# Kernel optimization log

Measured on AMD Instinct MI355X. Metric: run time of the kernel, lower is better.

## Reference

```python
import jax, jax.numpy as jnp
import numpy as np

D = 300
L = 5
NUM_ATOMS = 87  # MASK_ATOM_ID + 1
BN_EPS = 1e-5


def setup_inputs() -> dict:
    key = jax.random.key(0)
    ks = jax.random.split(key, 24)
    N, E, G = 100000, 250000, 4096
    s = 0.05
    inp = {
        'z': jax.random.randint(ks[0], (N,), 0, 86),
        'chirality': jax.random.uniform(ks[1], (N,), jnp.float32),
        'formal_charge': jax.random.normal(ks[2], (N,), jnp.float32),
        'edge_index': jax.random.randint(ks[3], (2, E), 0, N),
        'edge_attr': jax.random.normal(ks[4], (E, 3), jnp.float32),
        'batch': jnp.sort(jax.random.randint(ks[5], (N,), 0, G)),
        'num_graphs': G,
        # parameters
        'atom_emb': jax.random.normal(ks[6], (NUM_ATOMS, D), jnp.float32) * s,
        'nW1': jax.random.normal(ks[7], (2, D), jnp.float32) * s,
        'nb1': jnp.zeros((D,), jnp.float32),
        'nW2': jax.random.normal(ks[8], (D, D), jnp.float32) * s,
        'nb2': jnp.zeros((D,), jnp.float32),
        'eW1': jax.random.normal(ks[9], (3, D), jnp.float32) * s,
        'eb1': jnp.zeros((D,), jnp.float32),
        'eW2': jax.random.normal(ks[10], (D, D), jnp.float32) * s,
        'eb2': jnp.zeros((D,), jnp.float32),
        'mW1': jax.random.normal(ks[11], (L, D, D), jnp.float32) * s,
        'mb1': jnp.zeros((L, D), jnp.float32),
        'mW2': jax.random.normal(ks[12], (L, D, D), jnp.float32) * s,
        'mb2': jnp.zeros((L, D), jnp.float32),
        'gamma': jnp.ones((L, D), jnp.float32),
        'beta': jnp.zeros((L, D), jnp.float32),
        'pW': jax.random.normal(ks[13], (D, D), jnp.float32) * s,
        'pb': jnp.zeros((D,), jnp.float32),
    }
    return inp


def _mlp2(x, W1, b1, W2, b2):
    return jax.nn.relu(x @ W1 + b1) @ W2 + b2


def reference(z, chirality, formal_charge, edge_index, edge_attr, batch, num_graphs,
              atom_emb, nW1, nb1, nW2, nb2, eW1, eb1, eW2, eb2,
              mW1, mb1, mW2, mb2, gamma, beta, pW, pb):
    N = z.shape[0]
    # node features: atom embedding + projected (chirality, formal_charge)
    node_attr = jnp.stack([chirality, formal_charge], axis=-1)  # [N,2]
    x = atom_emb[z] + _mlp2(node_attr, nW1, nb1, nW2, nb2)      # [N,D]
    # edge features: encode 3-d bond attrs to D (edge_proj is Identity since dims match)
    e = _mlp2(edge_attr, eW1, eb1, eW2, eb2)                    # [E,D]
    src, dst = edge_index[0], edge_index[1]
    h = x
    for l in range(L):
        # GINEConv: mlp((1+eps)*x_i + sum_j relu(x_j + e_ij)), eps=0
        msg = jax.nn.relu(h[src] + e)                           # [E,D] gather
        agg = jax.ops.segment_sum(msg, dst, num_segments=N)     # [N,D] scatter-add
        h2 = _mlp2(h + agg, mW1[l], mb1[l], mW2[l], mb2[l])
        # BatchNorm1d (training stats over nodes, biased var)
        mu = jnp.mean(h2, axis=0)
        var = jnp.var(h2, axis=0)
        h2 = (h2 - mu) * jax.lax.rsqrt(var + BN_EPS) * gamma[l] + beta[l]
        h = jax.nn.relu(h2)
    # per-graph mean pooling
    sums = jax.ops.segment_sum(h, batch, num_segments=num_graphs)      # [G,D]
    counts = jax.ops.segment_sum(jnp.ones((N,), h.dtype), batch, num_segments=num_graphs)
    pooled = sums / jnp.maximum(counts, 1.0)[:, None]
    return pooled @ pW + pb
```

## Files before the change

### kernel.cpp

```cpp
#include <hip/hip_runtime.h>

#define DD 300
#define KP 320
#define WTR 384

typedef __attribute__((ext_vector_type(8))) short short8v;
typedef __attribute__((ext_vector_type(4))) float f32x4;

__device__ __forceinline__ float4 ld4(const float* p) { return *(const float4*)p; }

__device__ __forceinline__ unsigned short f2bf(float f) {
    unsigned int u = __float_as_uint(f);
    unsigned int r = (u + 0x7fffu + ((u >> 16) & 1u)) >> 16;
    return (unsigned short)r;
}
__device__ __forceinline__ float bf2f(unsigned short b) {
    return __uint_as_float(((unsigned int)b) << 16);
}

__device__ __forceinline__ void gload16(const void* g, void* l) {
    __builtin_amdgcn_global_load_lds(
        (const __attribute__((address_space(1))) unsigned int*)g,
        (__attribute__((address_space(3))) unsigned int*)l, 16, 0, 0);
}

__device__ __forceinline__ unsigned char f2e4(float f) {
    unsigned int u = __float_as_uint(f);
    unsigned int s = (u >> 24) & 0x80u;
    float a = __uint_as_float(u & 0x7fffffffu);
    if (a >= 448.f) return (unsigned char)(s | 0x7Eu);
    if (a < 0x1p-10f) return (unsigned char)s;
    int e = (int)((__float_as_uint(a) >> 23) & 0xFF) - 127;
    int q = (e >= -6) ? (e - 3) : -9;
    float scale = __uint_as_float((unsigned int)(127 - q) << 23);
    int m = __float2int_rn(a * scale);
    if (e >= -6) {
        if (m == 16) { m = 8; e += 1; }
        return (unsigned char)(s | ((unsigned int)(e + 7) << 3) | (unsigned int)(m - 8));
    } else {
        if (m == 8) return (unsigned char)(s | (1u << 3));
        return (unsigned char)(s | (unsigned int)m);
    }
}
__device__ __forceinline__ float e42f(unsigned char b) {
    unsigned int s = ((unsigned int)(b & 0x80u)) << 24;
    unsigned int ef = (b >> 3) & 0xFu, mf = b & 7u;
    float mag = (ef == 0) ? ((float)mf) * 0x1p-9f
                          : __uint_as_float(((ef + 120u) << 23) | (mf << 20));
    return __uint_as_float(__float_as_uint(mag) | s);
}

__global__ void prep_all(const float* __restrict__ nW2, const float* __restrict__ eW2,
                         const float* __restrict__ mW1, const float* __restrict__ mW2,
                         unsigned short* __restrict__ wt,
                         double* __restrict__ bnsum, double* __restrict__ bnsq)
{
    const int per = WTR * KP;
    int id = blockIdx.x * 256 + threadIdx.x;
    if (id < 12 * per) {
        int m = id / per, r = id - m * per;
        int col = r / KP, k = r - col * KP;
        const float* W = (m == 0) ? nW2 : (m == 1) ? eW2
                       : (m < 7) ? (mW1 + (size_t)(m - 2) * DD * DD)
                                 : (mW2 + (size_t)(m - 7) * DD * DD);
        float v = (col < DD && k < DD) ? W[(size_t)k * DD + col] : 0.f;
        unsigned short h = f2bf(v);
        wt[(size_t)m * 2 * per + (size_t)col * KP + k] = h;
        wt[(size_t)m * 2 * per + per + (size_t)col * KP + k] = f2bf(v - bf2f(h));
    } else if (id < 12 * per + DD) {
        int c = id - 12 * per;
        bnsum[c] = 0.0; bnsq[c] = 0.0;
    }
}

enum { MA_DMA2 = 0, MA_BF16 = 1, MA_NODE = 2, MA_EDGE = 3 };
enum { ME_RELU = 0, ME_BN = 1, ME_EMB = 2, ME_FP8 = 3 };

constexpr int TM = 128;
constexpr int TN = 128;
constexpr int TK = 32;
constexpr int KSTEPS = 10;

template<int AM, int EM>
__launch_bounds__(256)
__global__ void mgemm(const unsigned short* __restrict__ Aa,
                      const unsigned short* __restrict__ Ab,
                      const unsigned short* __restrict__ Bth,
                      const unsigned short* __restrict__ Btl,
                      const float* __restrict__ bias,
                      const float* __restrict__ W1,
                      const float* __restrict__ b1,
                      const int* __restrict__ zidx,
                      const float* __restrict__ emb,
                      const int* __restrict__ permpos,
                      void* __restrict__ Cv,
                      double* __restrict__ bnsum, double* __restrict__ bnsq,
                      int M)
{
    constexpr bool VSTAGE = (AM == MA_NODE || AM == MA_EDGE);
    constexpr int AP = VSTAGE ? 40 : 32;
    __shared__ unsigned short sAh[TM * AP];
    __shared__ unsigned short sBh[TN * 32];
    __shared__ unsigned short sBl[TN * 32];
    __shared__ unsigned short sA2[(AM == MA_DMA2) ? TM * 32 : 64];
    __shared__ unsigned short sAl[VSTAGE ? TM * 40 : 64];

    const int t    = threadIdx.x;
    const int col0 = blockIdx.x * TN;
    const int row0 = blockIdx.y * TM;
    const int lane = t & 63;
    const int wid  = t >> 6;
    const int wr   = wid >> 1;
    const int wc   = wid & 1;
    const int lr   = lane & 15;
    const int lk   = lane >> 4;

    const int arow = t >> 1;
    const int akq  = (t & 1) * 16;
    const int dmarow = lane >> 2;
    const int dmakq  = (lane & 3) * 8;
    const int wbase  = wid * 32;

    const int ga = row0 + arow;
    float f0 = 0.f, f1 = 0.f, f2 = 0.f;
    if (AM == MA_NODE && ga < M) {
        f0 = ((const float*)Aa)[ga]; f1 = ((const float*)Ab)[ga];
    }
    if (AM == MA_EDGE && ga < M) {
        const float* Af = (const float*)Aa;
        f0 = Af[(size_t)ga * 3 + 0];
        f1 = Af[(size_t)ga * 3 + 1];
        f2 = Af[(size_t)ga * 3 + 2];
    }

    f32x4 acc[4][4];
#pragma unroll
    for (int i = 0; i < 4; ++i)
#pragma unroll
        for (int j = 0; j < 4; ++j) acc[i][j] = (f32x4){0.f, 0.f, 0.f, 0.f};

    for (int ks = 0; ks < KSTEPS; ++ks) {
        const int k0 = ks * TK;
        __syncthreads();

#pragma unroll
        for (int i = 0; i < 2; ++i) {
            const int rb = wbase + i * 16;
            gload16(Bth + (size_t)(col0 + rb + dmarow) * KP + k0 + dmakq, &sBh[rb * 32]);
            gload16(Btl + (size_t)(col0 + rb + dmarow) * KP + k0 + dmakq, &sBl[rb * 32]);
        }

        if (AM == MA_DMA2) {
#pragma unroll
            for (int i = 0; i < 2; ++i) {
                const int rb = wbase + i * 16;
                gload16(Aa + (size_t)(row0 + rb + dmarow) * DD + k0 + dmakq, &sAh[rb * 32]);
                gload16(Ab + (size_t)(row0 + rb + dmarow) * DD + k0 + dmakq, &sA2[rb * 32]);
            }
        } else if (AM == MA_BF16) {
#pragma unroll
            for (int i = 0; i < 2; ++i) {
                const int rb = wbase + i * 16;
                gload16(Aa + (size_t)(row0 + rb + dmarow) * DD + k0 + dmakq, &sAh[rb * 32]);
            }
        } else {
            float v[16];
#pragma unroll
            for (int q = 0; q < 4; ++q) {
                const int k = k0 + akq + q * 4;
                if (ga < M && k < DD) {
                    float4 w0 = ld4(W1 + k);
                    float4 w1 = ld4(W1 + DD + k);
                    float4 bb = ld4(b1 + k);
                    if (AM == MA_NODE) {
                        v[q*4+0] = fmaxf(fmaf(f0, w0.x, fmaf(f1, w1.x, bb.x)), 0.f);
                        v[q*4+1] = fmaxf(fmaf(f0, w0.y, fmaf(f1, w1.y, bb.y)), 0.f);
                        v[q*4+2] = fmaxf(fmaf(f0, w0.z, fmaf(f1, w1.z, bb.z)), 0.f);
                        v[q*4+3] = fmaxf(fmaf(f0, w0.w, fmaf(f1, w1.w, bb.w)), 0.f);
                    } else {
                        float4 w2 = ld4(W1 + 2 * DD + k);
                        v[q*4+0] = fmaxf(f0*w0.x + f1*w1.x + f2*w2.x + bb.x, 0.f);
                        v[q*4+1] = fmaxf(f0*w0.y + f1*w1.y + f2*w2.y + bb.y, 0.f);
                        v[q*4+2] = fmaxf(f0*w0.z + f1*w1.z + f2*w2.z + bb.z, 0.f);
                        v[q*4+3] = fmaxf(f0*w0.w + f1*w1.w + f2*w2.w + bb.w, 0.f);
                    }
                } else {
                    v[q*4+0] = v[q*4+1] = v[q*4+2] = v[q*4+3] = 0.f;
                }
            }
#pragma unroll
            for (int q = 0; q < 4; ++q) {
                ushort4 hi, lo;
                hi.x = f2bf(v[q*4+0]); lo.x = f2bf(v[q*4+0] - bf2f(hi.x));
                hi.y = f2bf(v[q*4+1]); lo.y = f2bf(v[q*4+1] - bf2f(hi.y));
                hi.z = f2bf(v[q*4+2]); lo.z = f2bf(v[q*4+2] - bf2f(hi.z));
                hi.w = f2bf(v[q*4+3]); lo.w = f2bf(v[q*4+3] - bf2f(hi.w));
                *(ushort4*)&sAh[arow * AP + akq + q * 4] = hi;
                *(ushort4*)&sAl[arow * 40 + akq + q * 4] = lo;
            }
        }
        __syncthreads();

        short8v aH[4], aX[4], bH[4], bL[4];
#pragma unroll
        for (int f = 0; f < 4; ++f) {
            aH[f] = *(const short8v*)&sAh[(wr * 64 + f * 16 + lr) * AP + lk * 8];
            bH[f] = *(const short8v*)&sBh[(wc * 64 + f * 16 + lr) * 32 + lk * 8];
            bL[f] = *(const short8v*)&sBl[(wc * 64 + f * 16 + lr) * 32 + lk * 8];
            if constexpr (AM == MA_DMA2)
                aX[f] = *(const short8v*)&sA2[(wr * 64 + f * 16 + lr) * 32 + lk * 8];
            if constexpr (VSTAGE)
                aX[f] = *(const short8v*)&sAl[(wr * 64 + f * 16 + lr) * 40 + lk * 8];
        }
#pragma unroll
        for (int fi = 0; fi < 4; ++fi)
#pragma unroll
            for (int fj = 0; fj < 4; ++fj) {
                acc[fi][fj] = __builtin_amdgcn_mfma_f32_16x16x32_bf16(aH[fi], bH[fj], acc[fi][fj], 0, 0, 0);
                acc[fi][fj] = __builtin_amdgcn_mfma_f32_16x16x32_bf16(aH[fi], bL[fj], acc[fi][fj], 0, 0, 0);
                if constexpr (AM == MA_DMA2) {
                    acc[fi][fj] = __builtin_amdgcn_mfma_f32_16x16x32_bf16(aX[fi], bH[fj], acc[fi][fj], 0, 0, 0);
                    acc[fi][fj] = __builtin_amdgcn_mfma_f32_16x16x32_bf16(aX[fi], bL[fj], acc[fi][fj], 0, 0, 0);
                }
                if constexpr (VSTAGE)
                    acc[fi][fj] = __builtin_amdgcn_mfma_f32_16x16x32_bf16(aX[fi], bH[fj], acc[fi][fj], 0, 0, 0);
            }
    }

    float csum[4], csq[4];
#pragma unroll
    for (int j = 0; j < 4; ++j) { csum[j] = 0.f; csq[j] = 0.f; }

#pragma unroll
    for (int fi = 0; fi < 4; ++fi) {
#pragma unroll
        for (int i = 0; i < 4; ++i) {
            const int r = row0 + wr * 64 + fi * 16 + lk * 4 + i;
            if (r < M) {
                int zr = 0, pr = 0;
                if (EM == ME_EMB) zr = zidx[r];
                if (EM == ME_FP8) pr = permpos[r];
#pragma unroll
                for (int fj = 0; fj < 4; ++fj) {
                    const int c = col0 + wc * 64 + fj * 16 + lr;
                    if (c < DD) {
                        float v = acc[fi][fj][i] + bias[c];
                        if (EM == ME_RELU) v = fmaxf(v, 0.f);
                        if (EM == ME_EMB)  v += emb[(size_t)zr * DD + c];
                        if (EM == ME_FP8)
                            ((unsigned char*)Cv)[(size_t)pr * DD + c] = f2e4(v);
                        else
                            ((unsigned short*)Cv)[(size_t)r * DD + c] = f2bf(v);
                        if (EM == ME_BN) { csum[fj] += v; csq[fj] += v * v; }
                    }
                }
            }
        }
    }

    if (EM == ME_BN) {
#pragma unroll
        for (int fj = 0; fj < 4; ++fj) {
            csum[fj] += __shfl_xor(csum[fj], 16);
            csum[fj] += __shfl_xor(csum[fj], 32);
            csq[fj]  += __shfl_xor(csq[fj], 16);
            csq[fj]  += __shfl_xor(csq[fj], 32);
        }
        float* sRed = (float*)sAh;
        __syncthreads();
        if (lk == 0) {
#pragma unroll
            for (int fj = 0; fj < 4; ++fj)
                sRed[wr * TN + wc * 64 + fj * 16 + lr] = csum[fj];
        }
        __syncthreads();
        if (t < TN) {
            float s = sRed[t] + sRed[TN + t];
            const int c = col0 + t;
            if (c < DD) unsafeAtomicAdd(&bnsum[c], (double)s);
        }
        __syncthreads();
        if (lk == 0) {
#pragma unroll
            for (int fj = 0; fj < 4; ++fj)
                sRed[wr * TN + wc * 64 + fj * 16 + lr] = csq[fj];
        }
        __syncthreads();
        if (t < TN) {
            float s = sRed[t] + sRed[TN + t];
            const int c = col0 + t;
            if (c < DD) unsafeAtomicAdd(&bnsq[c], (double)s);
        }
    }
}

constexpr int GBM = 128;
constexpr int GBN = 128;
constexpr int GBK = 8;
constexpr int KPAD = 304;

__launch_bounds__(256)
__global__ void gemm_final(const float* __restrict__ Aa, const float* __restrict__ Bw,
                           const float* __restrict__ bias, float* __restrict__ C, int M)
{
    __shared__ float smem[2 * GBK * GBM];
    float* As = smem;
    float* Bs = smem + GBK * GBM;

    const int t    = threadIdx.x;
    const int tx   = t & 15;
    const int ty   = t >> 4;
    const int col0 = blockIdx.x * GBN;
    const int row0 = blockIdx.y * GBM;
    const int arow = t >> 1;
    const int akq  = (t & 1) << 2;
    const int brow = t >> 5;
    const int bnq  = (t & 31) << 2;
    const int ga   = row0 + arow;
    const int gb   = col0 + bnq;

    float acc[8][8];
#pragma unroll
    for (int i = 0; i < 8; ++i)
#pragma unroll
        for (int j = 0; j < 8; ++j) acc[i][j] = 0.f;

    for (int k0 = 0; k0 < KPAD; k0 += GBK) {
        float4 av = make_float4(0.f, 0.f, 0.f, 0.f);
        const int ka = k0 + akq;
        if (ga < M && ka < DD) av = ld4(Aa + (size_t)ga * DD + ka);
        As[(akq + 0) * GBM + arow] = av.x;
        As[(akq + 1) * GBM + arow] = av.y;
        As[(akq + 2) * GBM + arow] = av.z;
        As[(akq + 3) * GBM + arow] = av.w;

        float4 bv = make_float4(0.f, 0.f, 0.f, 0.f);
        const int kb = k0 + brow;
        if (kb < DD && gb < DD) bv = ld4(Bw + (size_t)kb * DD + gb);
        *(float4*)(Bs + brow * GBN + bnq) = bv;

        __syncthreads();
#pragma unroll
        for (int kk = 0; kk < GBK; ++kk) {
            float a[8], b[8];
            *(float4*)&a[0] = *(const float4*)(As + kk * GBM + 8 * ty);
            *(float4*)&a[4] = *(const float4*)(As + kk * GBM + 8 * ty + 4);
            *(float4*)&b[0] = *(const float4*)(Bs + kk * GBN + 8 * tx);
            *(float4*)&b[4] = *(const float4*)(Bs + kk * GBN + 8 * tx + 4);
#pragma unroll
            for (int i = 0; i < 8; ++i)
#pragma unroll
                for (int j = 0; j < 8; ++j)
                    acc[i][j] = fmaf(a[i], b[j], acc[i][j]);
        }
        __syncthreads();
    }

#pragma unroll
    for (int i = 0; i < 8; ++i) {
        const int r = row0 + 8 * ty + i;
        if (r < M) {
#pragma unroll
            for (int jq = 0; jq < 2; ++jq) {
                const int c = col0 + 8 * tx + 4 * jq;
                if (c < DD) {
                    float4 bb = ld4(bias + c);
                    *(float4*)(C + (size_t)r * DD + c) = make_float4(
                        acc[i][4*jq+0] + bb.x, acc[i][4*jq+1] + bb.y,
                        acc[i][4*jq+2] + bb.z, acc[i][4*jq+3] + bb.w);
                }
            }
        }
    }
}

__global__ void deg_kernel(const int* __restrict__ dst, int* __restrict__ deg, int E)
{
    int e = blockIdx.x * 256 + threadIdx.x;
    if (e < E) atomicAdd(&deg[dst[e]], 1);
}

__global__ void scan1(const int* __restrict__ deg, int* __restrict__ out,
                      int* __restrict__ bsum, int n)
{
    __shared__ int sh[256];
    const int t = threadIdx.x;
    const int base = blockIdx.x * 1024 + t * 4;
    int v0 = (base + 0 < n) ? deg[base + 0] : 0;
    int v1 = (base + 1 < n) ? deg[base + 1] : 0;
    int v2 = (base + 2 < n) ? deg[base + 2] : 0;
    int v3 = (base + 3 < n) ? deg[base + 3] : 0;
    const int s = v0 + v1 + v2 + v3;
    sh[t] = s;
    __syncthreads();
    for (int off = 1; off < 256; off <<= 1) {
        int x = (t >= off) ? sh[t - off] : 0;
        __syncthreads();
        sh[t] += x;
        __syncthreads();
    }
    int ex = sh[t] - s;
    if (base + 0 < n) out[base + 0] = ex; ex += v0;
    if (base + 1 < n) out[base + 1] = ex; ex += v1;
    if (base + 2 < n) out[base + 2] = ex; ex += v2;
    if (base + 3 < n) out[base + 3] = ex;
    if (t == 255) bsum[blockIdx.x] = sh[255];
}

__global__ void scan2(int* __restrict__ bsum, int nb, int* __restrict__ offs, int n, int E)
{
    __shared__ int sh[256];
    const int t = threadIdx.x;
    const int v = (t < nb) ? bsum[t] : 0;
    sh[t] = v;
    __syncthreads();
    for (int off = 1; off < 256; off <<= 1) {
        int x = (t >= off) ? sh[t - off] : 0;
        __syncthreads();
        sh[t] += x;
        __syncthreads();
    }
    if (t < nb) bsum[t] = sh[t] - v;
    if (t == 0) offs[n] = E;
}

__global__ void scan3(int* __restrict__ offs, const int* __restrict__ bsum,
                      int* __restrict__ cursor, int n)
{
    int i = blockIdx.x * 256 + threadIdx.x;
    if (i < n) {
        int v = offs[i] + bsum[i >> 10];
        offs[i] = v;
        cursor[i] = v;
    }
}

__global__ void fill_kernel(const int* __restrict__ src, const int* __restrict__ dst,
                            int* __restrict__ cursor, int* __restrict__ esrc,
                            int* __restrict__ permpos, int E)
{
    int e = blockIdx.x * 256 + threadIdx.x;
    if (e < E) {
        int d = dst[e];
        int pos = atomicAdd(&cursor[d], 1);
        esrc[pos] = src[e];
        permpos[e] = pos;
    }
}

__global__ void agg_kernel(const unsigned short* __restrict__ h,
                           const unsigned char* __restrict__ e,
                           const int* __restrict__ esrc, const int* __restrict__ offs,
                           unsigned short* __restrict__ agg, int N)
{
    const int node = blockIdx.x * 4 + (threadIdx.x >> 6);
    if (node >= N) return;
    const int lane = threadIdx.x & 63;
    const int beg = offs[node], end = offs[node + 1];
    for (int q = lane; q < 75; q += 64) {
        float4 s = make_float4(0.f, 0.f, 0.f, 0.f);
        for (int p = beg; p < end; ++p) {
            const int src = esrc[p];
            ushort4 hu = *(const ushort4*)(h + (size_t)src * DD + 4 * q);
            unsigned int eu = *(const unsigned int*)(e + (size_t)p * DD + 4 * q);
            s.x += fmaxf(bf2f(hu.x) + e42f((unsigned char)(eu & 0xFF)), 0.f);
            s.y += fmaxf(bf2f(hu.y) + e42f((unsigned char)((eu >> 8) & 0xFF)), 0.f);
            s.z += fmaxf(bf2f(hu.z) + e42f((unsigned char)((eu >> 16) & 0xFF)), 0.f);
            s.w += fmaxf(bf2f(hu.w) + e42f((unsigned char)(eu >> 24)), 0.f);
        }
        *(ushort4*)(agg + (size_t)node * DD + 4 * q) =
            make_ushort4(f2bf(s.x), f2bf(s.y), f2bf(s.z), f2bf(s.w));
    }
}

__global__ void bn_fin(double* __restrict__ bnsum, double* __restrict__ bnsq,
                       const float* __restrict__ gamma, const float* __restrict__ beta,
                       float* __restrict__ scale, float* __restrict__ shift, double invN)
{
    const int c = threadIdx.x;
    if (c < DD) {
        double mu = bnsum[c] * invN;
        double var = bnsq[c] * invN - mu * mu;
        double inv = 1.0 / sqrt(var + 1e-5);
        double g = (double)gamma[c];
        scale[c] = (float)(g * inv);
        shift[c] = (float)((double)beta[c] - mu * inv * g);
        bnsum[c] = 0.0;
        bnsq[c]  = 0.0;
    }
}

__global__ void bn_apply(const unsigned short* __restrict__ h2,
                         const float* __restrict__ scale, const float* __restrict__ shift,
                         unsigned short* __restrict__ h, int total4)
{
    int idx = blockIdx.x * 256 + threadIdx.x;
    if (idx >= total4) return;
    int q = idx % 75;
    ushort4 v4 = ((const ushort4*)h2)[idx];
    float4 sc = ld4(scale + 4 * q);
    float4 sh = ld4(shift + 4 * q);
    float r0 = fmaxf(fmaf(bf2f(v4.x), sc.x, sh.x), 0.f);
    float r1 = fmaxf(fmaf(bf2f(v4.y), sc.y, sh.y), 0.f);
    float r2 = fmaxf(fmaf(bf2f(v4.z), sc.z, sh.z), 0.f);
    float r3 = fmaxf(fmaf(bf2f(v4.w), sc.w, sh.w), 0.f);
    ((ushort4*)h)[idx] = make_ushort4(f2bf(r0), f2bf(r1), f2bf(r2), f2bf(r3));
}

__global__ void pool_kernel(const unsigned short* __restrict__ h, const int* __restrict__ batch,
                            float* __restrict__ pooled, int N)
{
    const int g = blockIdx.x;
    __shared__ int sb[2];
    if (threadIdx.x == 0) {
        int lo = 0, hi = N;
        while (lo < hi) { int m = (lo + hi) >> 1; if (batch[m] < g) lo = m + 1; else hi = m; }
        sb[0] = lo;
        lo = 0; hi = N;
        while (lo < hi) { int m = (lo + hi) >> 1; if (batch[m] < g + 1) lo = m + 1; else hi = m; }
        sb[1] = lo;
    }
    __syncthreads();
    const int beg = sb[0], end = sb[1];
    const float cnt = (float)(end - beg);
    for (int d = threadIdx.x; d < DD; d += 256) {
        float s = 0.f;
        for (int i = beg; i < end; ++i) s += bf2f(h[(size_t)i * DD + d]);
        pooled[(size_t)g * DD + d] = (end > beg) ? (s / cnt) : 0.f;
    }
}

__global__ void diag_fill(float* __restrict__ out, int n, float v)
{
    int i = blockIdx.x * 256 + threadIdx.x;
    if (i < n) out[i] = v;
}

extern "C" void kernel_launch(void* const* d_in, const int* in_sizes, int n_in,
                              void* d_out, int out_size, void* d_ws, size_t ws_size,
                              hipStream_t stream)
{
    const int N = in_sizes[0];
    const int E = in_sizes[3] / 2;
    const int G = out_size / DD;
    const int NPAD = (N + 127) & ~127;

    const int*   z     = (const int*)d_in[0];
    const float* chir  = (const float*)d_in[1];
    const float* fc    = (const float*)d_in[2];
    const int*   eidx  = (const int*)d_in[3];
    const float* eattr = (const float*)d_in[4];
    const int*   batch = (const int*)d_in[5];
    const float* aemb  = (const float*)d_in[7];
    const float* nW1   = (const float*)d_in[8];
    const float* nb1   = (const float*)d_in[9];
    const float* nW2   = (const float*)d_in[10];
    const float* nb2   = (const float*)d_in[11];
    const float* eW1   = (const float*)d_in[12];
    const float* eb1   = (const float*)d_in[13];
    const float* eW2   = (const float*)d_in[14];
    const float* eb2   = (const float*)d_in[15];
    const float* mW1   = (const float*)d_in[16];
    const float* mb1   = (const float*)d_in[17];
    const float* mW2   = (const float*)d_in[18];
    const float* mb2   = (const float*)d_in[19];
    const float* gamma = (const float*)d_in[20];
    const float* beta  = (const float*)d_in[21];
    const float* pW    = (const float*)d_in[22];
    const float* pb    = (const float*)d_in[23];
    float* out = (float*)d_out;

    size_t base = 0;
    auto A = [&](size_t b) -> size_t {
        size_t r = base; base += (b + 255) & ~(size_t)255; return r;
    };
    const size_t o_h    = A((size_t)NPAD * DD * 2 + 128);
    const size_t o_t    = A((size_t)NPAD * DD * 2 + 128);
    const size_t o_g    = A((size_t)NPAD * DD * 2 + 128);
    const size_t o_bns  = A(DD * 8);
    const size_t o_bnq  = A(DD * 8);
    const size_t o_scl  = A(DD * 4);
    const size_t o_shf  = A(DD * 4);
    const size_t o_offs = A((size_t)(N + 1) * 4);
    const size_t o_cur  = A((size_t)N * 4);
    const size_t o_bsum = A(1024 * 4);
    const size_t o_src  = A((size_t)E * 4);
    const size_t o_perm = A((size_t)E * 4);
    const size_t o_wt   = A((size_t)12 * 2 * WTR * KP * 2);
    const size_t o_e    = A((size_t)E * DD * 1);
    const size_t need = base;

    if (ws_size < need) {
        diag_fill<<<(out_size + 255) / 256, 256, 0, stream>>>(
            out, out_size, 10000.f + (float)(ws_size >> 20));
        return;
    }

    char* w = (char*)d_ws;
    unsigned short* h      = (unsigned short*)(w + o_h);
    unsigned short* tbuf   = (unsigned short*)(w + o_t);
    unsigned short* aggh2  = (unsigned short*)(w + o_g);
    double*         bnsum  = (double*)(w + o_bns);
    double*         bnsq   = (double*)(w + o_bnq);
    float*          scl    = (float*)(w + o_scl);
    float*          shf    = (float*)(w + o_shf);
    int*            offs   = (int*)(w + o_offs);
    int*            cursor = (int*)(w + o_cur);
    int*            bsum   = (int*)(w + o_bsum);
    int*            esrc   = (int*)(w + o_src);
    int*            permpos= (int*)(w + o_perm);
    unsigned short* wt     = (unsigned short*)(w + o_wt);
    unsigned char*  ebuf   = (unsigned char*)(w + o_e);
    float*          pooled = (float*)tbuf;

    const size_t per = (size_t)WTR * KP;
    auto wHI = [&](int m) { return wt + (size_t)m * 2 * per; };
    auto wLO = [&](int m) { return wt + (size_t)m * 2 * per + per; };

    const int* srcI = eidx;
    const int* dstI = eidx + E;

    const int ptot = 12 * WTR * KP + DD;
    prep_all<<<(ptot + 255) / 256, 256, 0, stream>>>(nW2, eW2, mW1, mW2, wt, bnsum, bnsq);

    hipMemsetAsync(cursor, 0, (size_t)N * 4, stream);
    deg_kernel<<<(E + 255) / 256, 256, 0, stream>>>(dstI, cursor, E);
    const int nb = (N + 1023) / 1024;
    scan1<<<nb, 256, 0, stream>>>(cursor, offs, bsum, N);
    scan2<<<1, 256, 0, stream>>>(bsum, nb, offs, N, E);
    scan3<<<(N + 255) / 256, 256, 0, stream>>>(offs, bsum, cursor, N);
    fill_kernel<<<(E + 255) / 256, 256, 0, stream>>>(srcI, dstI, cursor, esrc, permpos, E);

    const dim3 gN(3, (N + TM - 1) / TM);
    const dim3 gE(3, (E + TM - 1) / TM);
    const dim3 gG(3, (G + GBM - 1) / GBM);

    mgemm<MA_NODE, ME_EMB><<<gN, 256, 0, stream>>>(
        (const unsigned short*)chir, (const unsigned short*)fc, wHI(0), wLO(0), nb2,
        nW1, nb1, z, aemb, nullptr, h, nullptr, nullptr, N);
    mgemm<MA_EDGE, ME_FP8><<<gE, 256, 0, stream>>>(
        (const unsigned short*)eattr, nullptr, wHI(1), wLO(1), eb2,
        eW1, eb1, nullptr, nullptr, permpos, ebuf, nullptr, nullptr, E);

    for (int l = 0; l < 5; ++l) {
        agg_kernel<<<(N + 3) / 4, 256, 0, stream>>>(h, ebuf, esrc, offs, aggh2, N);
        mgemm<MA_DMA2, ME_RELU><<<gN, 256, 0, stream>>>(
            h, aggh2, wHI(2 + l), wLO(2 + l), mb1 + l * DD,
            nullptr, nullptr, nullptr, nullptr, nullptr, tbuf, nullptr, nullptr, N);
        mgemm<MA_BF16, ME_BN><<<gN, 256, 0, stream>>>(
            tbuf, nullptr, wHI(7 + l), wLO(7 + l), mb2 + l * DD,
            nullptr, nullptr, nullptr, nullptr, nullptr, aggh2, bnsum, bnsq, N);
        bn_fin<<<1, 320, 0, stream>>>(bnsum, bnsq, gamma + l * DD, beta + l * DD,
                                      scl, shf, 1.0 / (double)N);
        const int tot4 = N * 75;
        bn_apply<<<(tot4 + 255) / 256, 256, 0, stream>>>(aggh2, scl, shf, h, tot4);
    }

    pool_kernel<<<G, 256, 0, stream>>>(h, batch, pooled, N);
    gemm_final<<<gG, 256, 0, stream>>>(pooled, pW, pb, out, G);
}
```

Before: 2.727 ms.

## Double GEMM row tile to 256 with 512 threads and drop edge A-lo split

Raises the mgemm row tile from 128 to 256 rows and the block from 256 to 512 threads (8 waves), so each B weight tile fetched into LDS is reused across twice as many rows and loads are redistributed per wave. It also stops computing and multiplying the low bf16 residual of the staged A operand for the edge encoder, keeping it only for the node encoder, which removes one MFMA per tile pair there. The BN partial-sum reduction is widened to four row groups and node padding is rounded to 256. Larger blocks reduce the grid count and may lower occupancy, and dropping the A-lo term lowers edge-feature precision.

```diff
diff --git a/kernel.cpp b/kernel.cpp
--- a/kernel.cpp
+++ b/kernel.cpp
@@ -76,13 +76,13 @@
 enum { MA_DMA2 = 0, MA_BF16 = 1, MA_NODE = 2, MA_EDGE = 3 };
 enum { ME_RELU = 0, ME_BN = 1, ME_EMB = 2, ME_FP8 = 3 };
 
-constexpr int TM = 128;
+constexpr int TM = 256;
 constexpr int TN = 128;
 constexpr int TK = 32;
 constexpr int KSTEPS = 10;
 
 template<int AM, int EM>
-__launch_bounds__(256)
+__launch_bounds__(512)
 __global__ void mgemm(const unsigned short* __restrict__ Aa,
                       const unsigned short* __restrict__ Ab,
                       const unsigned short* __restrict__ Bth,
@@ -98,12 +98,13 @@
                       int M)
 {
     constexpr bool VSTAGE = (AM == MA_NODE || AM == MA_EDGE);
-    constexpr int AP = VSTAGE ? 40 : 32;
+    constexpr bool ALO    = (AM == MA_NODE);
+    constexpr int  AP     = VSTAGE ? 40 : 32;
     __shared__ unsigned short sAh[TM * AP];
     __shared__ unsigned short sBh[TN * 32];
     __shared__ unsigned short sBl[TN * 32];
     __shared__ unsigned short sA2[(AM == MA_DMA2) ? TM * 32 : 64];
-    __shared__ unsigned short sAl[VSTAGE ? TM * 40 : 64];
+    __shared__ unsigned short sAl[ALO ? TM * 40 : 64];
 
     const int t    = threadIdx.x;
     const int col0 = blockIdx.x * TN;
@@ -119,7 +120,8 @@
     const int akq  = (t & 1) * 16;
     const int dmarow = lane >> 2;
     const int dmakq  = (lane & 3) * 8;
-    const int wbase  = wid * 32;
+    const int wbA  = wid * 32;
+    const int wbB  = wid * 16;
 
     const int ga = row0 + arow;
     float f0 = 0.f, f1 = 0.f, f2 = 0.f;
@@ -143,24 +145,20 @@
         const int k0 = ks * TK;
         __syncthreads();
 
-#pragma unroll
-        for (int i = 0; i < 2; ++i) {
-            const int rb = wbase + i * 16;
-            gload16(Bth + (size_t)(col0 + rb + dmarow) * KP + k0 + dmakq, &sBh[rb * 32]);
-            gload16(Btl + (size_t)(col0 + rb + dmarow) * KP + k0 + dmakq, &sBl[rb * 32]);
-        }
+        gload16(Bth + (size_t)(col0 + wbB + dmarow) * KP + k0 + dmakq, &sBh[wbB * 32]);
+        gload16(Btl + (size_t)(col0 + wbB + dmarow) * KP + k0 + dmakq, &sBl[wbB * 32]);
 
         if (AM == MA_DMA2) {
 #pragma unroll
             for (int i = 0; i < 2; ++i) {
-                const int rb = wbase + i * 16;
+                const int rb = wbA + i * 16;
                 gload16(Aa + (size_t)(row0 + rb + dmarow) * DD + k0 + dmakq, &sAh[rb * 32]);
                 gload16(Ab + (size_t)(row0 + rb + dmarow) * DD + k0 + dmakq, &sA2[rb * 32]);
             }
         } else if (AM == MA_BF16) {
 #pragma unroll
             for (int i = 0; i < 2; ++i) {
-                const int rb = wbase + i * 16;
+                const int rb = wbA + i * 16;
                 gload16(Aa + (size_t)(row0 + rb + dmarow) * DD + k0 + dmakq, &sAh[rb * 32]);
             }
         } else {
@@ -190,13 +188,20 @@
             }
 #pragma unroll
             for (int q = 0; q < 4; ++q) {
-                ushort4 hi, lo;
-                hi.x = f2bf(v[q*4+0]); lo.x = f2bf(v[q*4+0] - bf2f(hi.x));
-                hi.y = f2bf(v[q*4+1]); lo.y = f2bf(v[q*4+1] - bf2f(hi.y));
-                hi.z = f2bf(v[q*4+2]); lo.z = f2bf(v[q*4+2] - bf2f(hi.z));
-                hi.w = f2bf(v[q*4+3]); lo.w = f2bf(v[q*4+3] - bf2f(hi.w));
+                ushort4 hi;
+                hi.x = f2bf(v[q*4+0]);
+                hi.y = f2bf(v[q*4+1]);
+                hi.z = f2bf(v[q*4+2]);
+                hi.w = f2bf(v[q*4+3]);
                 *(ushort4*)&sAh[arow * AP + akq + q * 4] = hi;
-                *(ushort4*)&sAl[arow * 40 + akq + q * 4] = lo;
+                if constexpr (ALO) {
+                    ushort4 lo;
+                    lo.x = f2bf(v[q*4+0] - bf2f(hi.x));
+                    lo.y = f2bf(v[q*4+1] - bf2f(hi.y));
+                    lo.z = f2bf(v[q*4+2] - bf2f(hi.z));
+                    lo.w = f2bf(v[q*4+3] - bf2f(hi.w));
+                    *(ushort4*)&sAl[arow * 40 + akq + q * 4] = lo;
+                }
             }
         }
         __syncthreads();
@@ -209,7 +214,7 @@
             bL[f] = *(const short8v*)&sBl[(wc * 64 + f * 16 + lr) * 32 + lk * 8];
             if constexpr (AM == MA_DMA2)
                 aX[f] = *(const short8v*)&sA2[(wr * 64 + f * 16 + lr) * 32 + lk * 8];
-            if constexpr (VSTAGE)
+            if constexpr (ALO)
                 aX[f] = *(const short8v*)&sAl[(wr * 64 + f * 16 + lr) * 40 + lk * 8];
         }
 #pragma unroll
@@ -222,7 +227,7 @@
                     acc[fi][fj] = __builtin_amdgcn_mfma_f32_16x16x32_bf16(aX[fi], bH[fj], acc[fi][fj], 0, 0, 0);
                     acc[fi][fj] = __builtin_amdgcn_mfma_f32_16x16x32_bf16(aX[fi], bL[fj], acc[fi][fj], 0, 0, 0);
                 }
-                if constexpr (VSTAGE)
+                if constexpr (ALO)
                     acc[fi][fj] = __builtin_amdgcn_mfma_f32_16x16x32_bf16(aX[fi], bH[fj], acc[fi][fj], 0, 0, 0);
             }
     }
@@ -275,7 +280,7 @@
         }
         __syncthreads();
         if (t < TN) {
-            float s = sRed[t] + sRed[TN + t];
+            float s = sRed[t] + sRed[TN + t] + sRed[2 * TN + t] + sRed[3 * TN + t];
             const int c = col0 + t;
             if (c < DD) unsafeAtomicAdd(&bnsum[c], (double)s);
         }
@@ -287,7 +292,7 @@
         }
         __syncthreads();
         if (t < TN) {
-            float s = sRed[t] + sRed[TN + t];
+            float s = sRed[t] + sRed[TN + t] + sRed[2 * TN + t] + sRed[3 * TN + t];
             const int c = col0 + t;
             if (c < DD) unsafeAtomicAdd(&bnsq[c], (double)s);
         }
@@ -543,7 +548,7 @@
     const int N = in_sizes[0];
     const int E = in_sizes[3] / 2;
     const int G = out_size / DD;
-    const int NPAD = (N + 127) & ~127;
+    const int NPAD = (N + 255) & ~255;
 
     const int*   z     = (const int*)d_in[0];
     const float* chir  = (const float*)d_in[1];
@@ -635,19 +640,19 @@
     const dim3 gE(3, (E + TM - 1) / TM);
     const dim3 gG(3, (G + GBM - 1) / GBM);
 
-    mgemm<MA_NODE, ME_EMB><<<gN, 256, 0, stream>>>(
+    mgemm<MA_NODE, ME_EMB><<<gN, 512, 0, stream>>>(
         (const unsigned short*)chir, (const unsigned short*)fc, wHI(0), wLO(0), nb2,
         nW1, nb1, z, aemb, nullptr, h, nullptr, nullptr, N);
-    mgemm<MA_EDGE, ME_FP8><<<gE, 256, 0, stream>>>(
+    mgemm<MA_EDGE, ME_FP8><<<gE, 512, 0, stream>>>(
         (const unsigned short*)eattr, nullptr, wHI(1), wLO(1), eb2,
         eW1, eb1, nullptr, nullptr, permpos, ebuf, nullptr, nullptr, E);
 
     for (int l = 0; l < 5; ++l) {
         agg_kernel<<<(N + 3) / 4, 256, 0, stream>>>(h, ebuf, esrc, offs, aggh2, N);
-        mgemm<MA_DMA2, ME_RELU><<<gN, 256, 0, stream>>>(
+        mgemm<MA_DMA2, ME_RELU><<<gN, 512, 0, stream>>>(
             h, aggh2, wHI(2 + l), wLO(2 + l), mb1 + l * DD,
             nullptr, nullptr, nullptr, nullptr, nullptr, tbuf, nullptr, nullptr, N);
-        mgemm<MA_BF16, ME_BN><<<gN, 256, 0, stream>>>(
+        mgemm<MA_BF16, ME_BN><<<gN, 512, 0, stream>>>(
             tbuf, nullptr, wHI(7 + l), wLO(7 + l), mb2 + l * DD,
             nullptr, nullptr, nullptr, nullptr, nullptr, aggh2, bnsum, bnsq, N);
         bn_fin<<<1, 320, 0, stream>>>(bnsum, bnsq, gamma + l * DD, beta + l * DD,
```

After: 2.625 ms. 1.04x faster.
